# Kernel tuning notes

Measured on AMD Instinct MI355X. Metric: run time of the kernel, lower is better.

Reference implementation:

```python
import jax, jax.numpy as jnp
import numpy as np

N = 256    # num_neurons
I = 784    # input_dim
H = 128    # hidden_dim
B = 256    # batch
E = 4096   # num edges (sparse topology, fan_out 16)


def setup_inputs() -> dict:
    key = jax.random.key(0)
    k0, k1, k2, k3, k4 = jax.random.split(key, 5)
    x = jax.random.normal(k0, (B, I), dtype=jnp.float32)
    # per-neuron linear weights/biases (AutonomicNeuron modeled as Linear(input_dim, hidden_dim))
    W = jax.random.normal(k1, (N, I, H), dtype=jnp.float32) * (1.0 / np.sqrt(I))
    b = jax.random.normal(k2, (N, H), dtype=jnp.float32) * 0.01
    edge_index = jax.random.randint(k3, (2, E), 0, N)  # (2, E) [src; tgt]
    edge_weights = jax.random.normal(k4, (E,), dtype=jnp.float32) * 0.01  # init scale in _init_*_topology
    return {"x": x, "W": W, "b": b, "edge_index": edge_index, "edge_weights": edge_weights}


def reference(x, W, b, edge_index, edge_weights):
    # per-neuron projection: h0[n] = x @ W[n] + b[n]  -> (N, B, H)
    h0 = jnp.einsum('bi,nih->nbh', x, W) + b[:, None, :]
    src = edge_index[0]
    tgt = edge_index[1]
    # sequential, order-dependent message passing (faithful to the Python edge loop):
    # h[tgt] <- h[tgt] + h[src] * w, using the CURRENT h[src]
    def step(h, sw):
        s, t, w = sw
        h = h.at[t].add(h[s] * w)
        return h, None
    h_final, _ = jax.lax.scan(step, h0, (src, tgt, edge_weights))
    # aggregate: mean over all neurons' hidden states -> (B, H)
    return h_final.mean(axis=0)
```

## Files before the change

kernel.cpp:

```cpp
#include <hip/hip_runtime.h>

#define EDGES 4096
#define NNODES 256

typedef unsigned short u16;

__global__ __launch_bounds__(256) void k1_coeff(const int* __restrict__ ei,
                                                const float* __restrict__ ew,
                                                float* __restrict__ c_out) {
    __shared__ __align__(16) char smem[59648];
    float* w_q    = (float*)(smem);
    u16*   s_e    = (u16*)  (smem + 16384);
    u16*   t_e    = (u16*)  (smem + 24576);
    float* rho    = (float*)(smem + 16384);
    u16*   id_q   = (u16*)  (smem + 32768);
    u16*   t_q    = (u16*)  (smem + 40960);
    float* sfx    = (float*)(smem + 32768);
    u16*   id_u   = (u16*)  (smem + 49152);
    u16*   start_q= (u16*)  (smem + 49152);
    int*   offs   = (int*)  (smem + 57344);
    int*   fillc  = (int*)  (smem + 58372);

    const int tid = threadIdx.x;

    for (int j = tid; j < EDGES; j += 256) {
        s_e[j] = (u16)ei[j];
        t_e[j] = (u16)ei[EDGES + j];
    }
    fillc[tid] = 0;
    __syncthreads();

    for (int j = tid; j < EDGES; j += 256) atomicAdd(&fillc[s_e[j]], 1);
    __syncthreads();

    if (tid == 0) offs[0] = 0;
    offs[tid + 1] = fillc[tid];
    __syncthreads();
    for (int d = 1; d < 256; d <<= 1) {
        int add = (tid >= d) ? offs[tid + 1 - d] : 0;
        __syncthreads();
        offs[tid + 1] += add;
        __syncthreads();
    }

    fillc[tid] = offs[tid];
    __syncthreads();

    for (int j = tid; j < EDGES; j += 256) {
        int pos = atomicAdd(&fillc[s_e[j]], 1);
        id_u[pos] = (u16)j;
    }
    __syncthreads();

    for (int j = tid; j < EDGES; j += 256) {
        int s = s_e[j];
        int lo = offs[s], hi = offs[s + 1];
        int rank = 0;
        for (int q = lo; q < hi; ++q) rank += (id_u[q] < j) ? 1 : 0;
        id_q[lo + rank] = (u16)j;
    }
    __syncthreads();

    for (int q = tid; q < EDGES; q += 256) {
        int e = id_q[q];
        w_q[q] = ew[e];
        t_q[q] = t_e[e];
    }
    __syncthreads();

    for (int q = tid; q < EDGES; q += 256) {
        int myid = id_q[q];
        int t = t_q[q];
        int lo = offs[t], hi = offs[t + 1];
        const int hi0 = hi;
        while (lo < hi) {
            int mid = (lo + hi) >> 1;
            if (id_q[mid] > myid) hi = mid; else lo = mid + 1;
        }
        start_q[q] = (lo < hi0) ? (u16)lo : (u16)0xFFFFu;
    }
    __syncthreads();

    for (int q = tid; q < EDGES; q += 256) rho[q] = 1.0f;
    __syncthreads();

    for (int pass = 0; pass < 5; ++pass) {
        for (int q = tid; q < EDGES; q += 256) sfx[q] = w_q[q] * rho[q];
        __syncthreads();
        {
            int lo = offs[tid], hi = offs[tid + 1];
            float run = 0.0f;
            for (int q = hi - 1; q >= lo; --q) { run += sfx[q]; sfx[q] = run; }
        }
        __syncthreads();
        for (int q = tid; q < EDGES; q += 256) {
            int st = start_q[q];
            rho[q] = 1.0f + ((st != 0xFFFF) ? sfx[st] : 0.0f);
        }
        __syncthreads();
    }

    {
        int lo = offs[tid], hi = offs[tid + 1];
        float acc = 0.0f;
        for (int q = lo; q < hi; ++q) acc += w_q[q] * rho[q];
        c_out[tid] = (1.0f + acc) * (1.0f / 256.0f);
    }
}

__global__ __launch_bounds__(256) void k2_wc(const float* __restrict__ W,
                                             const float* __restrict__ bvec,
                                             const float* __restrict__ c,
                                             float* __restrict__ Wc) {
    const int bx = blockIdx.x;
    const int p  = blockIdx.y;
    const int n0 = p * 32;

    if (bx == 98) {
        int tid = threadIdx.x;
        if (tid < 32) {
            const float4* b4 = (const float4*)bvec;
            float4 acc = make_float4(0.f, 0.f, 0.f, 0.f);
            #pragma unroll 8
            for (int n = 0; n < 32; ++n) {
                float cn = c[n0 + n];
                float4 v = b4[(n0 + n) * 32 + tid];
                acc.x += cn * v.x; acc.y += cn * v.y;
                acc.z += cn * v.z; acc.w += cn * v.w;
            }
            float* dst = Wc + 784 * 128 + tid * 4;
            atomicAdd(dst + 0, acc.x);
            atomicAdd(dst + 1, acc.y);
            atomicAdd(dst + 2, acc.z);
            atomicAdd(dst + 3, acc.w);
        }
        return;
    }

    const int j  = bx * 256 + threadIdx.x;
    const int i  = j >> 5;
    const int h4 = j & 31;
    const float4* W4 = (const float4*)W;
    float4 acc = make_float4(0.f, 0.f, 0.f, 0.f);
    #pragma unroll 8
    for (int n = 0; n < 32; ++n) {
        float cn = c[n0 + n];
        float4 v = W4[((size_t)(n0 + n) * 784 + i) * 32 + h4];
        acc.x += cn * v.x; acc.y += cn * v.y;
        acc.z += cn * v.z; acc.w += cn * v.w;
    }
    float* dst = Wc + i * 128 + h4 * 4;
    atomicAdd(dst + 0, acc.x);
    atomicAdd(dst + 1, acc.y);
    atomicAdd(dst + 2, acc.z);
    atomicAdd(dst + 3, acc.w);
}

__global__ __launch_bounds__(256) void k3_gemm(const float* __restrict__ x,
                                               const float* __restrict__ Wc,
                                               float* __restrict__ out) {
    const int bg = blockIdx.x;
    const int kc = blockIdx.y;
    const int i0 = kc * 49;
    __shared__ float xs[16][49];
    const int tid = threadIdx.x;

    for (int idx = tid; idx < 16 * 49; idx += 256) {
        int row = idx / 49, ii = idx - row * 49;
        xs[row][ii] = x[(bg * 16 + row) * 784 + i0 + ii];
    }
    __syncthreads();

    const int h  = tid & 127;
    const int bh = tid >> 7;
    float acc[8];
    #pragma unroll
    for (int j = 0; j < 8; ++j) acc[j] = 0.0f;

    #pragma unroll 7
    for (int ii = 0; ii < 49; ++ii) {
        float wv = Wc[(i0 + ii) * 128 + h];
        #pragma unroll
        for (int j = 0; j < 8; ++j) acc[j] += xs[bh * 8 + j][ii] * wv;
    }

    if (kc == 15) {
        float bch = Wc[784 * 128 + h];
        #pragma unroll
        for (int j = 0; j < 8; ++j) acc[j] += bch;
    }

    #pragma unroll
    for (int j = 0; j < 8; ++j)
        atomicAdd(&out[(bg * 16 + bh * 8 + j) * 128 + h], acc[j]);
}

extern "C" void kernel_launch(void* const* d_in, const int* in_sizes, int n_in,
                              void* d_out, int out_size, void* d_ws, size_t ws_size,
                              hipStream_t stream) {
    const float* x  = (const float*)d_in[0];
    const float* W  = (const float*)d_in[1];
    const float* bv = (const float*)d_in[2];
    const int*   ei = (const int*)d_in[3];
    const float* ew = (const float*)d_in[4];
    float* out = (float*)d_out;

    float* c_ws = (float*)d_ws;
    float* Wc   = (float*)d_ws + 256;

    hipMemsetAsync(out, 0, (size_t)256 * 128 * sizeof(float), stream);
    hipMemsetAsync(Wc, 0, (size_t)785 * 128 * sizeof(float), stream);

    k1_coeff<<<1, 256, 0, stream>>>(ei, ew, c_ws);
    k2_wc<<<dim3(99, 8), 256, 0, stream>>>(W, bv, c_ws, Wc);
    k3_gemm<<<dim3(16, 16), 256, 0, stream>>>(x, Wc, out);
}
```

Measured before the change: 217.5 us.

## Widen coefficient kernel to 1024 threads, shuffle scan, split W reduction finer

The single-block coefficient kernel now runs with 1024 threads. Its 256-entry offset scan is replaced by a one-wavefront shuffle scan, which removes many block-wide barriers. The W-weighted reduction grid doubles in the neuron dimension (16 neurons per block), giving more parallel blocks to stream the large W tensor, and W is read with nontemporal vector loads. The cost is twice as many atomic adds into Wc, and idle threads in the serial per-node phases of the first kernel.

```diff
diff --git a/kernel.cpp b/kernel.cpp
--- a/kernel.cpp
+++ b/kernel.cpp
@@ -4,10 +4,11 @@
 #define NNODES 256
 
 typedef unsigned short u16;
-
-__global__ __launch_bounds__(256) void k1_coeff(const int* __restrict__ ei,
-                                                const float* __restrict__ ew,
-                                                float* __restrict__ c_out) {
+typedef float f32x4 __attribute__((ext_vector_type(4)));
+
+__global__ __launch_bounds__(1024) void k1_coeff(const int* __restrict__ ei,
+                                                 const float* __restrict__ ew,
+                                                 float* __restrict__ c_out) {
     __shared__ __align__(16) char smem[59648];
     float* w_q    = (float*)(smem);
     u16*   s_e    = (u16*)  (smem + 16384);
@@ -23,36 +24,46 @@
 
     const int tid = threadIdx.x;
 
-    for (int j = tid; j < EDGES; j += 256) {
+    for (int j = tid; j < EDGES; j += 1024) {
         s_e[j] = (u16)ei[j];
         t_e[j] = (u16)ei[EDGES + j];
     }
-    fillc[tid] = 0;
-    __syncthreads();
-
-    for (int j = tid; j < EDGES; j += 256) atomicAdd(&fillc[s_e[j]], 1);
-    __syncthreads();
-
-    if (tid == 0) offs[0] = 0;
-    offs[tid + 1] = fillc[tid];
-    __syncthreads();
-    for (int d = 1; d < 256; d <<= 1) {
-        int add = (tid >= d) ? offs[tid + 1 - d] : 0;
-        __syncthreads();
-        offs[tid + 1] += add;
-        __syncthreads();
-    }
-
-    fillc[tid] = offs[tid];
-    __syncthreads();
-
-    for (int j = tid; j < EDGES; j += 256) {
+    if (tid < 256) fillc[tid] = 0;
+    __syncthreads();
+
+    for (int j = tid; j < EDGES; j += 1024) atomicAdd(&fillc[s_e[j]], 1);
+    __syncthreads();
+
+    if (tid < 64) {
+        const int base = tid << 2;
+        int c0 = fillc[base + 0], c1 = fillc[base + 1];
+        int c2 = fillc[base + 2], c3 = fillc[base + 3];
+        int s = c0 + c1 + c2 + c3;
+        int run = s;
+        #pragma unroll
+        for (int d = 1; d < 64; d <<= 1) {
+            int o = __shfl_up(run, d, 64);
+            if (tid >= d) run += o;
+        }
+        const int excl = run - s;
+        offs[base + 0] = excl;
+        offs[base + 1] = excl + c0;
+        offs[base + 2] = excl + c0 + c1;
+        offs[base + 3] = excl + c0 + c1 + c2;
+        if (tid == 63) offs[256] = run;
+    }
+    __syncthreads();
+
+    if (tid < 256) fillc[tid] = offs[tid];
+    __syncthreads();
+
+    for (int j = tid; j < EDGES; j += 1024) {
         int pos = atomicAdd(&fillc[s_e[j]], 1);
         id_u[pos] = (u16)j;
     }
     __syncthreads();
 
-    for (int j = tid; j < EDGES; j += 256) {
+    for (int j = tid; j < EDGES; j += 1024) {
         int s = s_e[j];
         int lo = offs[s], hi = offs[s + 1];
         int rank = 0;
@@ -61,14 +72,14 @@
     }
     __syncthreads();
 
-    for (int q = tid; q < EDGES; q += 256) {
+    for (int q = tid; q < EDGES; q += 1024) {
         int e = id_q[q];
         w_q[q] = ew[e];
         t_q[q] = t_e[e];
     }
     __syncthreads();
 
-    for (int q = tid; q < EDGES; q += 256) {
+    for (int q = tid; q < EDGES; q += 1024) {
         int myid = id_q[q];
         int t = t_q[q];
         int lo = offs[t], hi = offs[t + 1];
@@ -81,26 +92,26 @@
     }
     __syncthreads();
 
-    for (int q = tid; q < EDGES; q += 256) rho[q] = 1.0f;
+    for (int q = tid; q < EDGES; q += 1024) rho[q] = 1.0f;
     __syncthreads();
 
     for (int pass = 0; pass < 5; ++pass) {
-        for (int q = tid; q < EDGES; q += 256) sfx[q] = w_q[q] * rho[q];
+        for (int q = tid; q < EDGES; q += 1024) sfx[q] = w_q[q] * rho[q];
         __syncthreads();
-        {
+        if (tid < 256) {
             int lo = offs[tid], hi = offs[tid + 1];
             float run = 0.0f;
             for (int q = hi - 1; q >= lo; --q) { run += sfx[q]; sfx[q] = run; }
         }
         __syncthreads();
-        for (int q = tid; q < EDGES; q += 256) {
+        for (int q = tid; q < EDGES; q += 1024) {
             int st = start_q[q];
             rho[q] = 1.0f + ((st != 0xFFFF) ? sfx[st] : 0.0f);
         }
         __syncthreads();
     }
 
-    {
+    if (tid < 256) {
         int lo = offs[tid], hi = offs[tid + 1];
         float acc = 0.0f;
         for (int q = lo; q < hi; ++q) acc += w_q[q] * rho[q];
@@ -114,19 +125,18 @@
                                              float* __restrict__ Wc) {
     const int bx = blockIdx.x;
     const int p  = blockIdx.y;
-    const int n0 = p * 32;
+    const int n0 = p * 16;
 
     if (bx == 98) {
         int tid = threadIdx.x;
         if (tid < 32) {
-            const float4* b4 = (const float4*)bvec;
-            float4 acc = make_float4(0.f, 0.f, 0.f, 0.f);
-            #pragma unroll 8
-            for (int n = 0; n < 32; ++n) {
+            const f32x4* b4 = (const f32x4*)bvec;
+            f32x4 acc = {0.f, 0.f, 0.f, 0.f};
+            #pragma unroll
+            for (int n = 0; n < 16; ++n) {
                 float cn = c[n0 + n];
-                float4 v = b4[(n0 + n) * 32 + tid];
-                acc.x += cn * v.x; acc.y += cn * v.y;
-                acc.z += cn * v.z; acc.w += cn * v.w;
+                f32x4 v = b4[(n0 + n) * 32 + tid];
+                acc += v * cn;
             }
             float* dst = Wc + 784 * 128 + tid * 4;
             atomicAdd(dst + 0, acc.x);
@@ -140,14 +150,13 @@
     const int j  = bx * 256 + threadIdx.x;
     const int i  = j >> 5;
     const int h4 = j & 31;
-    const float4* W4 = (const float4*)W;
-    float4 acc = make_float4(0.f, 0.f, 0.f, 0.f);
-    #pragma unroll 8
-    for (int n = 0; n < 32; ++n) {
+    const f32x4* W4 = (const f32x4*)W;
+    f32x4 acc = {0.f, 0.f, 0.f, 0.f};
+    #pragma unroll
+    for (int n = 0; n < 16; ++n) {
         float cn = c[n0 + n];
-        float4 v = W4[((size_t)(n0 + n) * 784 + i) * 32 + h4];
-        acc.x += cn * v.x; acc.y += cn * v.y;
-        acc.z += cn * v.z; acc.w += cn * v.w;
+        f32x4 v = __builtin_nontemporal_load(&W4[((size_t)(n0 + n) * 784 + i) * 32 + h4]);
+        acc += v * cn;
     }
     float* dst = Wc + i * 128 + h4 * 4;
     atomicAdd(dst + 0, acc.x);
@@ -211,7 +220,7 @@
     hipMemsetAsync(out, 0, (size_t)256 * 128 * sizeof(float), stream);
     hipMemsetAsync(Wc, 0, (size_t)785 * 128 * sizeof(float), stream);
 
-    k1_coeff<<<1, 256, 0, stream>>>(ei, ew, c_ws);
-    k2_wc<<<dim3(99, 8), 256, 0, stream>>>(W, bv, c_ws, Wc);
+    k1_coeff<<<1, 1024, 0, stream>>>(ei, ew, c_ws);
+    k2_wc<<<dim3(99, 16), 256, 0, stream>>>(W, bv, c_ws, Wc);
     k3_gemm<<<dim3(16, 16), 256, 0, stream>>>(x, Wc, out);
 }
```

Measured after the change: 201.6 us. 1.08x faster.
